# Kernel tuning notes

Hardware: AMD Instinct MI355X
Metric: run time of the kernel (lower is better)

Reference implementation:

```python
import jax, jax.numpy as jnp
import numpy as np

DIM = 128
N_ENT = 500000
N_REL = 500
GAMMA = 12.0
EPS = 1e-12  # F.normalize eps


def l2norm(x):
    n = jnp.sqrt(jnp.sum(x * x, axis=-1, keepdims=True))
    return x / jnp.maximum(n, EPS)


def setup_inputs() -> dict:
    key = jax.random.key(0)
    k1, k2, k3, k4, k5, k6 = jax.random.split(key, 6)
    B = 16384
    h = jax.random.randint(k1, (B,), 0, N_ENT)
    r = jax.random.randint(k2, (B,), 0, 2 * N_REL)
    t = jax.random.randint(k3, (B,), 0, N_ENT)
    # xavier_uniform-like init
    def xav(k, shape):
        bound = float(np.sqrt(6.0 / (shape[0] + shape[1])))
        return jax.random.uniform(k, shape, jnp.float32, -bound, bound)
    ent_w = xav(k4, (N_ENT, DIM))
    rel_w = xav(k5, (N_REL, DIM))
    mat_w = xav(k6, (N_REL, DIM * DIM))
    return {"h": h, "r": r, "t": t, "ent_w": ent_w, "rel_w": rel_w, "mat_w": mat_w}


def reference(h, r, t, ent_w, rel_w, mat_w):
    # r indexes into doubled tables: [mat; mat] and [rel; -rel]
    mat_full = jnp.concatenate([mat_w, mat_w], axis=0)          # [2R, D*D]
    rel_full = jnp.concatenate([rel_w, -rel_w], axis=0)         # [2R, D]
    mat = mat_full[r].reshape(-1, DIM, DIM)                      # [B, D, D]
    rv = l2norm(rel_full[r])                                     # [B, D]
    hv = l2norm(ent_w[h])                                        # [B, D]
    tv = l2norm(ent_w[t])                                        # [B, D]
    # _transfer: (1,D) @ (D,D) -> (D,), then L2 normalize
    hp = l2norm(jnp.einsum('bd,bde->be', hv, mat))
    tp = l2norm(jnp.einsum('bd,bde->be', tv, mat))
    dist = hp + rv - tp
    score = GAMMA - jnp.sqrt(jnp.sum(dist * dist, axis=-1))      # p=2 norm
    return score
```

## Files before the change

### kernel.cpp

```cpp
#include <hip/hip_runtime.h>

#define DIM   128
#define N_REL 500
#define GAMMA 12.0f
#define EPS   1e-12f
#define SPLIT 2
#define MAXS  96

__device__ __forceinline__ float waveSum(float v) {
#pragma unroll
    for (int off = 32; off > 0; off >>= 1)
        v += __shfl_xor(v, off, 64);
    return v;
}

__global__ __launch_bounds__(256, 4) void k_fused(
    const int* __restrict__ h, const int* __restrict__ r, const int* __restrict__ t,
    const float* __restrict__ ent_w, const float* __restrict__ rel_w,
    const float* __restrict__ mat_w, float* __restrict__ out, int B)
{
    const int rel  = blockIdx.x / SPLIT;
    const int sp   = blockIdx.x % SPLIT;
    const int tid  = threadIdx.x;
    const int eg   = tid & 31;
    const int dc   = tid >> 5;
    const int e    = tid & 127;
    const int vsel = tid >> 7;
    const int lane = tid & 63;
    const int wv   = tid >> 6;

    const float4* __restrict__ M4 = (const float4*)(mat_w + (size_t)rel * DIM * DIM);
    float4 Mreg[16];
#pragma unroll
    for (int dd = 0; dd < 16; ++dd)
        Mreg[dd] = M4[(dc * 16 + dd) * 32 + eg];

    __shared__ int   s_b[MAXS], s_h[MAXS], s_t[MAXS];
    __shared__ float s_sg[MAXS];
    __shared__ int   lcnt;
    __shared__ float srv[DIM];
    __shared__ float sv[4][DIM];
    __shared__ float part[8][4][DIM];
    __shared__ float ppv[4][DIM];
    __shared__ float wsA[4], wsB[4], wsD[4];

    if (tid == 0) lcnt = 0;
    __syncthreads();

    const int lo = (B * sp) / SPLIT, hiEnd = (B * (sp + 1)) / SPLIT;
    for (int i = lo + tid; i < hiEnd; i += 256) {
        int ri = r[i];
        int mi = (ri >= N_REL) ? ri - N_REL : ri;
        if (mi == rel) {
            int p = atomicAdd(&lcnt, 1);
            if (p < MAXS) {
                s_b[p]  = i;
                s_h[p]  = h[i];
                s_t[p]  = t[i];
                s_sg[p] = (ri >= N_REL) ? -1.0f : 1.0f;
            }
        }
    }

    float rv = (vsel == 0) ? rel_w[(size_t)rel * DIM + e] : 0.0f;
    float rp = waveSum(rv * rv);
    if (lane == 0) wsA[wv] = rp;
    __syncthreads();
    const int n = min(lcnt, MAXS);
    if (n == 0) return;
    if (vsel == 0)
        srv[e] = rv / fmaxf(sqrtf(wsA[0] + wsA[1]), EPS);
    __syncthreads();

    for (int s0 = 0; s0 < n; s0 += 2) {
        const bool two = (s0 + 1 < n);

        {
            int row0 = vsel ? s_t[s0] : s_h[s0];
            sv[vsel][e] = ent_w[(size_t)row0 * DIM + e];
            if (two) {
                int row1 = vsel ? s_t[s0 + 1] : s_h[s0 + 1];
                sv[2 + vsel][e] = ent_w[(size_t)row1 * DIM + e];
            }
        }
        __syncthreads();

        float4 a0 = make_float4(0.f,0.f,0.f,0.f), a1 = a0, a2 = a0, a3 = a0;
#pragma unroll
        for (int dd = 0; dd < 16; ++dd) {
            const float4 m = Mreg[dd];
            const float x0 = sv[0][dc*16+dd], x1 = sv[1][dc*16+dd];
            const float x2 = sv[2][dc*16+dd], x3 = sv[3][dc*16+dd];
            a0.x += x0*m.x; a0.y += x0*m.y; a0.z += x0*m.z; a0.w += x0*m.w;
            a1.x += x1*m.x; a1.y += x1*m.y; a1.z += x1*m.z; a1.w += x1*m.w;
            a2.x += x2*m.x; a2.y += x2*m.y; a2.z += x2*m.z; a2.w += x2*m.w;
            a3.x += x3*m.x; a3.y += x3*m.y; a3.z += x3*m.z; a3.w += x3*m.w;
        }
        *(float4*)&part[dc][0][4*eg] = a0;
        *(float4*)&part[dc][1][4*eg] = a1;
        *(float4*)&part[dc][2][4*eg] = a2;
        *(float4*)&part[dc][3][4*eg] = a3;
        __syncthreads();

        float v0 = 0.f, v1 = 0.f;
#pragma unroll
        for (int k = 0; k < 8; ++k) {
            v0 += part[k][vsel][e];
            v1 += part[k][vsel + 2][e];
        }
        ppv[vsel][e]     = v0;
        ppv[vsel + 2][e] = v1;
        const float n0 = waveSum(v0 * v0);
        const float n1 = waveSum(v1 * v1);
        if (lane == 0) { wsA[wv] = n0; wsB[wv] = n1; }
        __syncthreads();

        const int   smp  = wv >> 1;
        const float hs   = smp ? (wsB[0] + wsB[1]) : (wsA[0] + wsA[1]);
        const float ts   = smp ? (wsB[2] + wsB[3]) : (wsA[2] + wsA[3]);
        const float hinv = 1.0f / fmaxf(sqrtf(hs), EPS);
        const float tinv = 1.0f / fmaxf(sqrtf(ts), EPS);
        const float sg   = s_sg[s0 + smp < n ? s0 + smp : s0];
        const float d    = ppv[2*smp][e] * hinv + sg * srv[e] - ppv[2*smp+1][e] * tinv;
        const float dq   = waveSum(d * d);
        if (lane == 0) wsD[wv] = dq;
        __syncthreads();

        if (tid == 0)        out[s_b[s0]]     = GAMMA - sqrtf(wsD[0] + wsD[1]);
        if (tid == 1 && two) out[s_b[s0 + 1]] = GAMMA - sqrtf(wsD[2] + wsD[3]);
    }
}

extern "C" void kernel_launch(void* const* d_in, const int* in_sizes, int n_in,
                              void* d_out, int out_size, void* d_ws, size_t ws_size,
                              hipStream_t stream) {
    const int*   h     = (const int*)d_in[0];
    const int*   r     = (const int*)d_in[1];
    const int*   t     = (const int*)d_in[2];
    const float* ent_w = (const float*)d_in[3];
    const float* rel_w = (const float*)d_in[4];
    const float* mat_w = (const float*)d_in[5];
    float*       out   = (float*)d_out;
    const int B = in_sizes[0];

    k_fused<<<N_REL * SPLIT, 256, 0, stream>>>(h, r, t, ent_w, rel_w, mat_w, out, B);
}
```

Baseline: 363.2 us.

## Hold full matrix column per thread, drop cross-thread partial reduction, prefetch entity rows

Measured after the change: 838.7 us. +130.9%, slower.

```diff
diff --git a/kernel.cpp b/kernel.cpp
--- a/kernel.cpp
+++ b/kernel.cpp
@@ -14,120 +14,128 @@
     return v;
 }
 
-__global__ __launch_bounds__(256, 4) void k_fused(
+__global__ __launch_bounds__(128, 2) void k_fused(
     const int* __restrict__ h, const int* __restrict__ r, const int* __restrict__ t,
     const float* __restrict__ ent_w, const float* __restrict__ rel_w,
     const float* __restrict__ mat_w, float* __restrict__ out, int B)
 {
     const int rel  = blockIdx.x / SPLIT;
     const int sp   = blockIdx.x % SPLIT;
-    const int tid  = threadIdx.x;
-    const int eg   = tid & 31;
-    const int dc   = tid >> 5;
-    const int e    = tid & 127;
-    const int vsel = tid >> 7;
-    const int lane = tid & 63;
-    const int wv   = tid >> 6;
+    const int e    = threadIdx.x;
+    const int lane = e & 63;
+    const int wv   = e >> 6;
 
-    const float4* __restrict__ M4 = (const float4*)(mat_w + (size_t)rel * DIM * DIM);
-    float4 Mreg[16];
+    float Mc[DIM];
+    const float* __restrict__ Mp = mat_w + (size_t)rel * DIM * DIM + e;
 #pragma unroll
-    for (int dd = 0; dd < 16; ++dd)
-        Mreg[dd] = M4[(dc * 16 + dd) * 32 + eg];
+    for (int d = 0; d < DIM; ++d)
+        Mc[d] = Mp[(size_t)d * DIM];
 
-    __shared__ int   s_b[MAXS], s_h[MAXS], s_t[MAXS];
-    __shared__ float s_sg[MAXS];
-    __shared__ int   lcnt;
-    __shared__ float srv[DIM];
-    __shared__ float sv[4][DIM];
-    __shared__ float part[8][4][DIM];
-    __shared__ float ppv[4][DIM];
-    __shared__ float wsA[4], wsB[4], wsD[4];
+    __shared__ int    s_b[MAXS], s_h[MAXS], s_t[MAXS];
+    __shared__ float  s_sg[MAXS];
+    __shared__ int    lcnt;
+    __shared__ float4 sx4[DIM];
+    __shared__ float  wsN[2][4];
+    __shared__ float  wsD[2][2];
+    __shared__ float  relh[2];
 
-    if (tid == 0) lcnt = 0;
+    if (e == 0) lcnt = 0;
     __syncthreads();
 
     const int lo = (B * sp) / SPLIT, hiEnd = (B * (sp + 1)) / SPLIT;
-    for (int i = lo + tid; i < hiEnd; i += 256) {
-        int ri = r[i];
-        int mi = (ri >= N_REL) ? ri - N_REL : ri;
-        if (mi == rel) {
-            int p = atomicAdd(&lcnt, 1);
-            if (p < MAXS) {
-                s_b[p]  = i;
-                s_h[p]  = h[i];
-                s_t[p]  = t[i];
-                s_sg[p] = (ri >= N_REL) ? -1.0f : 1.0f;
+#pragma unroll 1
+    for (int i = lo + e * 4; i < hiEnd; i += 128 * 4) {
+        const int4 q = *(const int4*)(r + i);
+        const int rr[4] = { q.x, q.y, q.z, q.w };
+#pragma unroll
+        for (int j = 0; j < 4; ++j) {
+            const int ri = rr[j];
+            const int mi = (ri >= N_REL) ? ri - N_REL : ri;
+            if (mi == rel) {
+                const int p = atomicAdd(&lcnt, 1);
+                if (p < MAXS) {
+                    s_b[p]  = i + j;
+                    s_h[p]  = h[i + j];
+                    s_t[p]  = t[i + j];
+                    s_sg[p] = (ri >= N_REL) ? -1.0f : 1.0f;
+                }
             }
         }
     }
 
-    float rv = (vsel == 0) ? rel_w[(size_t)rel * DIM + e] : 0.0f;
-    float rp = waveSum(rv * rv);
-    if (lane == 0) wsA[wv] = rp;
+    const float rvv = rel_w[(size_t)rel * DIM + e];
+    {
+        const float rp = waveSum(rvv * rvv);
+        if (lane == 0) relh[wv] = rp;
+    }
     __syncthreads();
     const int n = min(lcnt, MAXS);
     if (n == 0) return;
-    if (vsel == 0)
-        srv[e] = rv / fmaxf(sqrtf(wsA[0] + wsA[1]), EPS);
-    __syncthreads();
+    const float srv_e = rvv / fmaxf(sqrtf(relh[0] + relh[1]), EPS);
+
+    const int i1 = (1 < n) ? 1 : 0;
+    float ph0 = ent_w[(size_t)s_h[0]  * DIM + e];
+    float pt0 = ent_w[(size_t)s_t[0]  * DIM + e];
+    float ph1 = ent_w[(size_t)s_h[i1] * DIM + e];
+    float pt1 = ent_w[(size_t)s_t[i1] * DIM + e];
 
     for (int s0 = 0; s0 < n; s0 += 2) {
         const bool two = (s0 + 1 < n);
 
-        {
-            int row0 = vsel ? s_t[s0] : s_h[s0];
-            sv[vsel][e] = ent_w[(size_t)row0 * DIM + e];
-            if (two) {
-                int row1 = vsel ? s_t[s0 + 1] : s_h[s0 + 1];
-                sv[2 + vsel][e] = ent_w[(size_t)row1 * DIM + e];
+        sx4[e] = make_float4(ph0, pt0, ph1, pt1);
+        __syncthreads();
+
+        if (s0 + 2 < n) {
+            const int a = s0 + 2;
+            const int b = (s0 + 3 < n) ? s0 + 3 : a;
+            ph0 = ent_w[(size_t)s_h[a] * DIM + e];
+            pt0 = ent_w[(size_t)s_t[a] * DIM + e];
+            ph1 = ent_w[(size_t)s_h[b] * DIM + e];
+            pt1 = ent_w[(size_t)s_t[b] * DIM + e];
+        }
+
+        float hp0 = 0.f, tp0 = 0.f, hp1 = 0.f, tp1 = 0.f;
+#pragma unroll
+        for (int k = 0; k < 8; ++k) {
+            float c0 = 0.f, c1 = 0.f, c2 = 0.f, c3 = 0.f;
+#pragma unroll
+            for (int dd = 0; dd < 16; ++dd) {
+                const float4 x = sx4[k * 16 + dd];
+                const float  m = Mc[k * 16 + dd];
+                c0 += x.x * m;
+                c1 += x.y * m;
+                c2 += x.z * m;
+                c3 += x.w * m;
             }
+            hp0 += c0; tp0 += c1; hp1 += c2; tp1 += c3;
+        }
+
+        const float nh0 = waveSum(hp0 * hp0);
+        const float nt0 = waveSum(tp0 * tp0);
+        const float nh1 = waveSum(hp1 * hp1);
+        const float nt1 = waveSum(tp1 * tp1);
+        if (lane == 0) {
+            wsN[wv][0] = nh0; wsN[wv][1] = nt0;
+            wsN[wv][2] = nh1; wsN[wv][3] = nt1;
         }
         __syncthreads();
 
-        float4 a0 = make_float4(0.f,0.f,0.f,0.f), a1 = a0, a2 = a0, a3 = a0;
-#pragma unroll
-        for (int dd = 0; dd < 16; ++dd) {
-            const float4 m = Mreg[dd];
-            const float x0 = sv[0][dc*16+dd], x1 = sv[1][dc*16+dd];
-            const float x2 = sv[2][dc*16+dd], x3 = sv[3][dc*16+dd];
-            a0.x += x0*m.x; a0.y += x0*m.y; a0.z += x0*m.z; a0.w += x0*m.w;
-            a1.x += x1*m.x; a1.y += x1*m.y; a1.z += x1*m.z; a1.w += x1*m.w;
-            a2.x += x2*m.x; a2.y += x2*m.y; a2.z += x2*m.z; a2.w += x2*m.w;
-            a3.x += x3*m.x; a3.y += x3*m.y; a3.z += x3*m.z; a3.w += x3*m.w;
-        }
-        *(float4*)&part[dc][0][4*eg] = a0;
-        *(float4*)&part[dc][1][4*eg] = a1;
-        *(float4*)&part[dc][2][4*eg] = a2;
-        *(float4*)&part[dc][3][4*eg] = a3;
+        const float hinv0 = 1.0f / fmaxf(sqrtf(wsN[0][0] + wsN[1][0]), EPS);
+        const float tinv0 = 1.0f / fmaxf(sqrtf(wsN[0][1] + wsN[1][1]), EPS);
+        const float hinv1 = 1.0f / fmaxf(sqrtf(wsN[0][2] + wsN[1][2]), EPS);
+        const float tinv1 = 1.0f / fmaxf(sqrtf(wsN[0][3] + wsN[1][3]), EPS);
+        const float sg0   = s_sg[s0];
+        const float sg1   = s_sg[two ? s0 + 1 : s0];
+
+        const float d0  = hp0 * hinv0 + sg0 * srv_e - tp0 * tinv0;
+        const float d1  = hp1 * hinv1 + sg1 * srv_e - tp1 * tinv1;
+        const float dq0 = waveSum(d0 * d0);
+        const float dq1 = waveSum(d1 * d1);
+        if (lane == 0) { wsD[wv][0] = dq0; wsD[wv][1] = dq1; }
         __syncthreads();
 
-        float v0 = 0.f, v1 = 0.f;
-#pragma unroll
-        for (int k = 0; k < 8; ++k) {
-            v0 += part[k][vsel][e];
-            v1 += part[k][vsel + 2][e];
-        }
-        ppv[vsel][e]     = v0;
-        ppv[vsel + 2][e] = v1;
-        const float n0 = waveSum(v0 * v0);
-        const float n1 = waveSum(v1 * v1);
-        if (lane == 0) { wsA[wv] = n0; wsB[wv] = n1; }
-        __syncthreads();
-
-        const int   smp  = wv >> 1;
-        const float hs   = smp ? (wsB[0] + wsB[1]) : (wsA[0] + wsA[1]);
-        const float ts   = smp ? (wsB[2] + wsB[3]) : (wsA[2] + wsA[3]);
-        const float hinv = 1.0f / fmaxf(sqrtf(hs), EPS);
-        const float tinv = 1.0f / fmaxf(sqrtf(ts), EPS);
-        const float sg   = s_sg[s0 + smp < n ? s0 + smp : s0];
-        const float d    = ppv[2*smp][e] * hinv + sg * srv[e] - ppv[2*smp+1][e] * tinv;
-        const float dq   = waveSum(d * d);
-        if (lane == 0) wsD[wv] = dq;
-        __syncthreads();
-
-        if (tid == 0)        out[s_b[s0]]     = GAMMA - sqrtf(wsD[0] + wsD[1]);
-        if (tid == 1 && two) out[s_b[s0 + 1]] = GAMMA - sqrtf(wsD[2] + wsD[3]);
+        if (e == 0)        out[s_b[s0]]     = GAMMA - sqrtf(wsD[0][0] + wsD[1][0]);
+        if (e == 1 && two) out[s_b[s0 + 1]] = GAMMA - sqrtf(wsD[0][1] + wsD[1][1]);
     }
 }
 
@@ -143,5 +151,5 @@
     float*       out   = (float*)d_out;
     const int B = in_sizes[0];
 
-    k_fused<<<N_REL * SPLIT, 256, 0, stream>>>(h, r, t, ent_w, rel_w, mat_w, out, B);
+    k_fused<<<N_REL * SPLIT, 128, 0, stream>>>(h, r, t, ent_w, rel_w, mat_w, out, B);
 }
```
